# Kernel tuning notes

Hardware: AMD Instinct MI355X
Metric: run time of the kernel (lower is better)

## Reference

```python
import jax, jax.numpy as jnp
import numpy as np

H, M, K, V, F, L = 8, 1024, 128, 128, 4096, 6
B, Q, T = 4, 1024, 1024
EPS = 1e-5


def layer_norm(x, g, b):
    mu = jnp.mean(x, axis=-1, keepdims=True)
    var = jnp.var(x, axis=-1, keepdims=True)
    return (x - mu) * jax.lax.rsqrt(var + EPS) * g + b


def mha(qinput, kvinput, qmask, tmask, qtmask, wq, wk, wv, wo):
    # qinput: bqm, kvinput: btm, masks 1 = ignore
    logits_mask = jnp.maximum(tmask[:, None, :], qtmask)  # bqt
    query = jnp.einsum('hmd,bqm->bhqd', wq, qinput)
    key = jnp.einsum('hmd,btm->bhtd', wk, kvinput)
    val = jnp.einsum('hmd,btm->bhtd', wv, kvinput)
    alogit = jnp.einsum('bhqd,bhtd->bhqt', query, key) + logits_mask[:, None] * -1e6
    att = jax.nn.softmax(alogit * (1.0 / np.sqrt(K)), axis=3)
    pre = jnp.einsum('bhqt,bhtd->bhqd', att, val)
    out = jnp.einsum('hdm,bhqd->bqm', wo, pre)
    return out * (1.0 - qmask[:, :, None])


def ffn(x, qmask, w1, b1, w2, b2):
    s = jax.nn.relu(jnp.einsum('mf,bqm->bqf', w1, x) + b1)
    out = jnp.einsum('fm,bqf->bqm', w2, s) + b2
    return out * (1.0 - qmask[:, :, None])


def setup_inputs() -> dict:
    key = jax.random.key(0)
    ks = jax.random.split(key, 16)
    mscale, fscale, vscale = M ** -0.5, F ** -0.5, V ** -0.5
    d = {
        'enc_out': jax.random.normal(ks[0], (B, T, M), jnp.float32),
        'x': jax.random.normal(ks[1], (B, Q, M), jnp.float32),
        'position_mask': jnp.zeros((B, Q), jnp.float32),
        'qt_self_mask': jnp.broadcast_to(
            (jnp.arange(Q)[:, None] < jnp.arange(Q)[None, :]).astype(jnp.float32),
            (B, Q, Q)),
        'qt_cross_mask': jnp.zeros((B, Q, T), jnp.float32),
        # self-attention params, stacked over layers
        'swq': jax.random.normal(ks[2], (L, H, M, K), jnp.float32) * mscale,
        'swk': jax.random.normal(ks[3], (L, H, M, K), jnp.float32) * mscale,
        'swv': jax.random.normal(ks[4], (L, H, M, V), jnp.float32) * mscale,
        'swo': jax.random.normal(ks[5], (L, H, V, M), jnp.float32) * vscale,
        # cross-attention params
        'cwq': jax.random.normal(ks[6], (L, H, M, K), jnp.float32) * mscale,
        'cwk': jax.random.normal(ks[7], (L, H, M, K), jnp.float32) * mscale,
        'cwv': jax.random.normal(ks[8], (L, H, M, V), jnp.float32) * mscale,
        'cwo': jax.random.normal(ks[9], (L, H, V, M), jnp.float32) * vscale,
        # FFN params
        'w1': jax.random.normal(ks[10], (L, M, F), jnp.float32) * mscale,
        'b1': jnp.zeros((L, F), jnp.float32),
        'w2': jax.random.normal(ks[11], (L, F, M), jnp.float32) * fscale,
        'b2': jnp.zeros((L, M), jnp.float32),
        # LayerNorm params
        'ln1_g': jnp.ones((L, M), jnp.float32), 'ln1_b': jnp.zeros((L, M), jnp.float32),
        'ln2_g': jnp.ones((L, M), jnp.float32), 'ln2_b': jnp.zeros((L, M), jnp.float32),
        'ln3_g': jnp.ones((L, M), jnp.float32), 'ln3_b': jnp.zeros((L, M), jnp.float32),
    }
    return d


def reference(enc_out, x, position_mask, qt_self_mask, qt_cross_mask,
              swq, swk, swv, swo, cwq, cwk, cwv, cwo,
              w1, b1, w2, b2, ln1_g, ln1_b, ln2_g, ln2_b, ln3_g, ln3_b):
    zeros_t = jnp.zeros((enc_out.shape[0], enc_out.shape[1]), x.dtype)
    h = x
    for l in range(L):
        n1 = layer_norm(h, ln1_g[l], ln1_b[l])
        a1 = mha(n1, n1, position_mask, position_mask, qt_self_mask,
                 swq[l], swk[l], swv[l], swo[l])
        h1 = h + a1
        n2 = layer_norm(h1, ln2_g[l], ln2_b[l])
        a2 = mha(n2, enc_out, position_mask, zeros_t, qt_cross_mask,
                 cwq[l], cwk[l], cwv[l], cwo[l])
        h2 = h1 + a2
        n3 = layer_norm(h2, ln3_g[l], ln3_b[l])
        h = h2 + ffn(n3, position_mask, w1[l], b1[l], w2[l], b2[l])
    return h
```

## Files before the change

kernel.cpp:

```cpp
#include <hip/hip_runtime.h>
#include <math.h>

#define NL 6
#define NH 8
#define MD 1024
#define HD 128
#define FF 4096
#define NB 4
#define NQ 1024
#define NT 1024
#define ROWS (NB*NQ)

typedef __attribute__((ext_vector_type(8))) short bf16x8;
typedef __attribute__((ext_vector_type(4))) float f32x4;

__device__ __forceinline__ unsigned short f2bf(float f) {
    unsigned int u = __float_as_uint(f);
    u += 0x7fffu + ((u >> 16) & 1u);
    return (unsigned short)(u >> 16);
}

__device__ __forceinline__ void load16_lds(const unsigned short* g, unsigned short* l) {
    __builtin_amdgcn_global_load_lds(
        (const __attribute__((address_space(1))) unsigned int*)g,
        (__attribute__((address_space(3))) unsigned int*)l, 16, 0, 0);
}

__global__ __launch_bounds__(256) void ln_kernel(
    const float* __restrict__ x, unsigned short* __restrict__ y,
    const float* __restrict__ g, const float* __restrict__ b)
{
    __shared__ float sdata[8];
    int row = blockIdx.x;
    int tid = threadIdx.x;
    const float* xr = x + (size_t)row * MD;
    float4 v = ((const float4*)xr)[tid];
    float s = v.x + v.y + v.z + v.w;
    #pragma unroll
    for (int o = 32; o > 0; o >>= 1) s += __shfl_down(s, o, 64);
    if ((tid & 63) == 0) sdata[tid >> 6] = s;
    __syncthreads();
    if (tid == 0) sdata[4] = sdata[0] + sdata[1] + sdata[2] + sdata[3];
    __syncthreads();
    float mean = sdata[4] * (1.0f / MD);
    float4 d = make_float4(v.x - mean, v.y - mean, v.z - mean, v.w - mean);
    float sq = d.x*d.x + d.y*d.y + d.z*d.z + d.w*d.w;
    #pragma unroll
    for (int o = 32; o > 0; o >>= 1) sq += __shfl_down(sq, o, 64);
    __syncthreads();
    if ((tid & 63) == 0) sdata[tid >> 6] = sq;
    __syncthreads();
    if (tid == 0) sdata[4] = sdata[0] + sdata[1] + sdata[2] + sdata[3];
    __syncthreads();
    float var = sdata[4] * (1.0f / MD);
    float rstd = rsqrtf(var + 1e-5f);
    float4 g4 = ((const float4*)g)[tid];
    float4 b4 = ((const float4*)b)[tid];
    ushort4 o;
    o.x = f2bf(d.x * rstd * g4.x + b4.x);
    o.y = f2bf(d.y * rstd * g4.y + b4.y);
    o.z = f2bf(d.z * rstd * g4.z + b4.z);
    o.w = f2bf(d.w * rstd * g4.w + b4.w);
    *(ushort4*)(y + (size_t)row * MD + tid * 4) = o;
}

__global__ __launch_bounds__(256) void cast_bf16(
    const float* __restrict__ x, unsigned short* __restrict__ y)
{
    int i = blockIdx.x * 256 + threadIdx.x;
    float4 v = ((const float4*)x)[i];
    ushort4 o;
    o.x = f2bf(v.x); o.y = f2bf(v.y); o.z = f2bf(v.z); o.w = f2bf(v.w);
    ((ushort4*)y)[i] = o;
}

__global__ __launch_bounds__(256) void transpose_cast(
    const float* __restrict__ X, unsigned short* __restrict__ Y, int R, int C)
{
    __shared__ float tile[32][33];
    int bz = blockIdx.z;
    int r0 = blockIdx.y * 32, c0 = blockIdx.x * 32;
    const float* Xb = X + (size_t)bz * R * C;
    unsigned short* Yb = Y + (size_t)bz * R * C;
    int tx = threadIdx.x & 31, ty = threadIdx.x >> 5;
    #pragma unroll
    for (int i = 0; i < 4; i++)
        tile[ty + i*8][tx] = Xb[(size_t)(r0 + ty + i*8) * C + c0 + tx];
    __syncthreads();
    #pragma unroll
    for (int i = 0; i < 4; i++)
        Yb[(size_t)(c0 + ty + i*8) * R + r0 + tx] = f2bf(tile[tx][ty + i*8]);
}

#define BKK 64
#define ASZ (128 * BKK)

__device__ __forceinline__ void stage_tiles(
    unsigned short* As, unsigned short* Bs,
    const unsigned short* __restrict__ A, int lda,
    const unsigned short* __restrict__ BT, int ldb,
    int row0, int col0, int kt)
{
    int tid = threadIdx.x;
    #pragma unroll
    for (int it = 0; it < 4; it++) {
        int idx = it * 256 + tid;
        int r = idx >> 3, c = (idx & 7) * 8;
        load16_lds(A + (size_t)(row0 + r) * lda + kt + c, &As[idx * 8]);
    }
    #pragma unroll
    for (int it = 0; it < 4; it++) {
        int idx = it * 256 + tid;
        int r = idx >> 3, c = (idx & 7) * 8;
        load16_lds(BT + (size_t)(col0 + r) * ldb + kt + c, &Bs[idx * 8]);
    }
}

__device__ __forceinline__ void gemm_body(
    unsigned short* As, unsigned short* Bs,
    const unsigned short* __restrict__ A, int lda,
    const unsigned short* __restrict__ BT, int ldb,
    void* __restrict__ Cout, int ldc, int Kdim, int flags,
    const float* __restrict__ bias, int row0, int col0)
{
    int tid = threadIdx.x;
    int lane = tid & 63;
    int wave = tid >> 6;
    int mr = (wave & 1) * 64;
    int nc = (wave >> 1) * 64;
    int lr = lane & 15;
    int quad = lane >> 4;

    f32x4 acc[4][4];
    #pragma unroll
    for (int i = 0; i < 4; i++)
        #pragma unroll
        for (int j = 0; j < 4; j++) acc[i][j] = (f32x4)0.0f;

    const int NKi = Kdim >> 6;
    stage_tiles(As, Bs, A, lda, BT, ldb, row0, col0, 0);
    __syncthreads();

    for (int k = 0; k < NKi; k++) {
        unsigned short* cA = As + (k & 1) * ASZ;
        unsigned short* cB = Bs + (k & 1) * ASZ;
        if (k + 1 < NKi)
            stage_tiles(As + ((k + 1) & 1) * ASZ, Bs + ((k + 1) & 1) * ASZ,
                        A, lda, BT, ldb, row0, col0, (k + 1) * BKK);
        #pragma unroll
        for (int ks = 0; ks < 2; ks++) {
            bf16x8 af[4], bfr[4];
            #pragma unroll
            for (int i = 0; i < 4; i++)
                af[i] = *(const bf16x8*)&cA[(mr + i*16 + lr) * BKK + ks*32 + quad*8];
            #pragma unroll
            for (int j = 0; j < 4; j++)
                bfr[j] = *(const bf16x8*)&cB[(nc + j*16 + lr) * BKK + ks*32 + quad*8];
            #pragma unroll
            for (int i = 0; i < 4; i++)
                #pragma unroll
                for (int j = 0; j < 4; j++)
                    acc[i][j] = __builtin_amdgcn_mfma_f32_16x16x32_bf16(
                        af[i], bfr[j], acc[i][j], 0, 0, 0);
        }
        __syncthreads();
    }

    float bvj[4];
    if (flags & 4) {
        #pragma unroll
        for (int j = 0; j < 4; j++) bvj[j] = bias[col0 + nc + j*16 + lr];
    } else {
        #pragma unroll
        for (int j = 0; j < 4; j++) bvj[j] = 0.0f;
    }

    if (flags & 1) {
        unsigned short* V = (unsigned short*)Cout;
        #pragma unroll
        for (int i = 0; i < 4; i++) {
            int grow0 = row0 + mr + i*16 + quad*4;
            int bb = grow0 >> 10, tt = grow0 & 1023;
            #pragma unroll
            for (int j = 0; j < 4; j++) {
                int gcol = col0 + nc + j*16 + lr;
                int hh = gcol >> 7, dd = gcol & 127;
                ushort4 pk;
                pk.x = f2bf(acc[i][j][0]); pk.y = f2bf(acc[i][j][1]);
                pk.z = f2bf(acc[i][j][2]); pk.w = f2bf(acc[i][j][3]);
                *(ushort4*)(V + (((size_t)(bb*NH + hh)*HD + dd) * NT + tt)) = pk;
            }
        }
    } else if (flags & 2) {
        float* Cf = (float*)Cout;
        #pragma unroll
        for (int i = 0; i < 4; i++) {
            int grow0 = row0 + mr + i*16 + quad*4;
            #pragma unroll
            for (int j = 0; j < 4; j++) {
                int gcol = col0 + nc + j*16 + lr;
                #pragma unroll
                for (int r = 0; r < 4; r++) {
                    float v = acc[i][j][r] + bvj[j];
                    atomicAdd(&Cf[(size_t)(grow0 + r) * ldc + gcol], v);
                }
            }
        }
    } else {
        unsigned short* Cb = (unsigned short*)Cout;
        #pragma unroll
        for (int i = 0; i < 4; i++) {
            int grow0 = row0 + mr + i*16 + quad*4;
            #pragma unroll
            for (int j = 0; j < 4; j++) {
                int gcol = col0 + nc + j*16 + lr;
                #pragma unroll
                for (int r = 0; r < 4; r++) {
                    float v = acc[i][j][r] + bvj[j];
                    if (flags & 8) v = fmaxf(v, 0.0f);
                    Cb[(size_t)(grow0 + r) * ldc + gcol] = f2bf(v);
                }
            }
        }
    }
}

__global__ __launch_bounds__(256) void gemm_bf16(
    const unsigned short* __restrict__ A, int lda,
    const unsigned short* __restrict__ BT, int ldb,
    void* __restrict__ Cout, int ldc, int Kper, int flags,
    const float* __restrict__ bias)
{
    __shared__ unsigned short As[2 * ASZ];
    __shared__ unsigned short Bs[2 * ASZ];
    int row0 = blockIdx.y * 128, col0 = blockIdx.x * 128;
    int kbase = blockIdx.z * Kper;
    if (blockIdx.z) flags &= ~4;
    gemm_body(As, Bs, A + kbase, lda, BT + kbase, ldb, Cout, ldc,
              Kper, flags, bias, row0, col0);
}

__global__ __launch_bounds__(256) void gemm_qkv(
    const unsigned short* __restrict__ Aq,
    const unsigned short* __restrict__ Akv,
    const unsigned short* __restrict__ BTq,
    const unsigned short* __restrict__ BTk,
    const unsigned short* __restrict__ BTv,
    unsigned short* __restrict__ qb,
    unsigned short* __restrict__ kb,
    unsigned short* __restrict__ vbt)
{
    __shared__ unsigned short As[2 * ASZ];
    __shared__ unsigned short Bs[2 * ASZ];
    int w = blockIdx.x >> 3;
    int col0 = (blockIdx.x & 7) * 128;
    int row0 = blockIdx.y * 128;
    const unsigned short* A  = (w == 0) ? Aq : Akv;
    const unsigned short* BT = (w == 0) ? BTq : (w == 1) ? BTk : BTv;
    void* C  = (w == 0) ? (void*)qb : (w == 1) ? (void*)kb : (void*)vbt;
    int flags = (w == 2) ? 1 : 0;
    gemm_body(As, Bs, A, MD, BT, MD, C, MD, MD, flags, nullptr, row0, col0);
}

#define KVB 64

__global__ __launch_bounds__(256) void attn_mfma(
    const unsigned short* __restrict__ qb, const unsigned short* __restrict__ kb,
    const unsigned short* __restrict__ vbt, unsigned short* __restrict__ pr,
    int causal)
{
    __shared__ unsigned short Qs[64 * 136];
    __shared__ unsigned short Ks[64 * 136];
    __shared__ unsigned short Vs[128 * 72];
    __shared__ unsigned short Ps[4 * 16 * 72];

    int tid = threadIdx.x;
    int lane = tid & 63, wave = tid >> 6;
    int lr = lane & 15, quad = lane >> 4;

    int qt, bh;
    if (causal) {
        int bid = blockIdx.x + 16 * blockIdx.y;
        int half = bid >> 8, j = bid & 255;
        qt = half ? (15 - (j & 15)) : (j & 15);
        bh = (half << 4) | (j >> 4);
    } else {
        qt = blockIdx.x; bh = blockIdx.y;
    }
    int b = bh >> 3, h = bh & 7;
    int q0 = qt * 64;
    const float scale = 0.08838834764831845f;

    const unsigned short* kbase = kb + (size_t)(b * NT) * MD + h * HD;
    const unsigned short* vbase = vbt + (size_t)((b * NH + h) * HD) * NT;

    uint4 kreg[4], vreg[4];
    #pragma unroll
    for (int it = 0; it < 4; it++) {
        int idx = it * 256 + tid;
        int r = idx >> 4, c = (idx & 15) * 8;
        kreg[it] = *(const uint4*)(kbase + (size_t)r * MD + c);
    }
    #pragma unroll
    for (int it = 0; it < 4; it++) {
        int idx = it * 256 + tid;
        int r = idx >> 3, c = (idx & 7) * 8;
        vreg[it] = *(const uint4*)(vbase + (size_t)r * NT + c);
    }

    #pragma unroll
    for (int it = 0; it < 4; it++) {
        int idx = it * 256 + tid;
        int r = idx >> 4, c = (idx & 15) * 8;
        *(uint4*)&Qs[r * 136 + c] =
            *(const uint4*)(qb + (size_t)(b*NQ + q0 + r) * MD + h*HD + c);
    }
    __syncthreads();
    bf16x8 aq[4];
    #pragma unroll
    for (int dk = 0; dk < 4; dk++)
        aq[dk] = *(const bf16x8*)&Qs[(wave*16 + lr) * 136 + dk*32 + quad*8];

    f32x4 acc[8];
    #pragma unroll
    for (int n = 0; n < 8; n++) acc[n] = (f32x4)0.0f;
    float m_run[4], l_run[4];
    #pragma unroll
    for (int r = 0; r < 4; r++) { m_run[r] = -1e30f; l_run[r] = 0.0f; }

    unsigned short* Pw = &Ps[wave * 16 * 72];
    int nch = causal ? (qt + 1) : (NT / KVB);
    int grow_base = q0 + wave*16 + quad*4;

    for (int tc = 0; tc < nch; tc++) {
        __syncthreads();
        #pragma unroll
        for (int it = 0; it < 4; it++) {
            int idx = it * 256 + tid;
            int r = idx >> 4, c = (idx & 15) * 8;
            *(uint4*)&Ks[r * 136 + c] = kreg[it];
        }
        #pragma unroll
        for (int it = 0; it < 4; it++) {
            int idx = it * 256 + tid;
            int r = idx >> 3, c = (idx & 7) * 8;
            *(uint4*)&Vs[r * 72 + c] = vreg[it];
        }
        if (tc + 1 < nch) {
            int t0n = (tc + 1) * KVB;
            #pragma unroll
            for (int it = 0; it < 4; it++) {
                int idx = it * 256 + tid;
                int r = idx >> 4, c = (idx & 15) * 8;
                kreg[it] = *(const uint4*)(kbase + (size_t)(t0n + r) * MD + c);
            }
            #pragma unroll
            for (int it = 0; it < 4; it++) {
                int idx = it * 256 + tid;
                int r = idx >> 3, c = (idx & 7) * 8;
                vreg[it] = *(const uint4*)(vbase + (size_t)r * NT + t0n + c);
            }
        }
        __syncthreads();

        int t0 = tc * KVB;

        f32x4 s[4];
        #pragma unroll
        for (int kt = 0; kt < 4; kt++) s[kt] = (f32x4)0.0f;
        __builtin_amdgcn_s_setprio(1);
        #pragma unroll
        for (int dk = 0; dk < 4; dk++) {
            #pragma unroll
            for (int kt = 0; kt < 4; kt++) {
                bf16x8 bk = *(const bf16x8*)&Ks[(kt*16 + lr) * 136 + dk*32 + quad*8];
                s[kt] = __builtin_amdgcn_mfma_f32_16x16x32_bf16(aq[dk], bk, s[kt], 0, 0, 0);
            }
        }
        __builtin_amdgcn_s_setprio(0);

        #pragma unroll
        for (int r = 0; r < 4; r++) {
            float v[4];
            #pragma unroll
            for (int kt = 0; kt < 4; kt++) {
                float x = s[kt][r] * scale;
                if (causal && (t0 + kt*16 + lr > grow_base + r)) x = -1e30f;
                v[kt] = x;
            }
            float mx = fmaxf(fmaxf(v[0], v[1]), fmaxf(v[2], v[3]));
            #pragma unroll
            for (int off = 1; off < 16; off <<= 1)
                mx = fmaxf(mx, __shfl_xor(mx, off));
            mx = fmaxf(mx, m_run[r]);
            float alpha = __expf(m_run[r] - mx);
            float psum = 0.0f;
            #pragma unroll
            for (int kt = 0; kt < 4; kt++) {
                float p = __expf(v[kt] - mx);
                Pw[(quad*4 + r) * 72 + kt*16 + lr] = f2bf(p);
                psum += p;
            }
            #pragma unroll
            for (int off = 1; off < 16; off <<= 1)
                psum += __shfl_xor(psum, off);
            l_run[r] = l_run[r] * alpha + psum;
            m_run[r] = mx;
            #pragma unroll
            for (int n = 0; n < 8; n++) acc[n][r] *= alpha;
        }

        bf16x8 ap0 = *(const bf16x8*)&Pw[lr * 72 + quad * 8];
        bf16x8 ap1 = *(const bf16x8*)&Pw[lr * 72 + 32 + quad * 8];
        __builtin_amdgcn_s_setprio(1);
        #pragma unroll
        for (int n = 0; n < 8; n++) {
            bf16x8 bv0 = *(const bf16x8*)&Vs[(n*16 + lr) * 72 + quad * 8];
            bf16x8 bv1 = *(const bf16x8*)&Vs[(n*16 + lr) * 72 + 32 + quad * 8];
            acc[n] = __builtin_amdgcn_mfma_f32_16x16x32_bf16(ap0, bv0, acc[n], 0, 0, 0);
            acc[n] = __builtin_amdgcn_mfma_f32_16x16x32_bf16(ap1, bv1, acc[n], 0, 0, 0);
        }
        __builtin_amdgcn_s_setprio(0);
    }

    float linv[4];
    #pragma unroll
    for (int r = 0; r < 4; r++) linv[r] = 1.0f / l_run[r];
    #pragma unroll
    for (int n = 0; n < 8; n++) {
        int gcol = h*HD + n*16 + lr;
        #pragma unroll
        for (int r = 0; r < 4; r++) {
            int grow = q0 + wave*16 + quad*4 + r;
            pr[(size_t)(b*NQ + grow) * MD + gcol] = f2bf(acc[n][r] * linv[r]);
        }
    }
}

extern "C" void kernel_launch(void* const* d_in, const int* in_sizes, int n_in,
                              void* d_out, int out_size, void* d_ws, size_t ws_size,
                              hipStream_t stream)
{
    const float* enc  = (const float*)d_in[0];
    const float* x    = (const float*)d_in[1];
    const float* swq  = (const float*)d_in[5];
    const float* swk  = (const float*)d_in[6];
    const float* swv  = (const float*)d_in[7];
    const float* swo  = (const float*)d_in[8];
    const float* cwq  = (const float*)d_in[9];
    const float* cwk  = (const float*)d_in[10];
    const float* cwv  = (const float*)d_in[11];
    const float* cwo  = (const float*)d_in[12];
    const float* w1   = (const float*)d_in[13];
    const float* b1   = (const float*)d_in[14];
    const float* w2   = (const float*)d_in[15];
    const float* b2   = (const float*)d_in[16];
    const float* ln1g = (const float*)d_in[17];
    const float* ln1b = (const float*)d_in[18];
    const float* ln2g = (const float*)d_in[19];
    const float* ln2b = (const float*)d_in[20];
    const float* ln3g = (const float*)d_in[21];
    const float* ln3b = (const float*)d_in[22];

    float* h = (float*)d_out;
    unsigned short* u = (unsigned short*)d_ws;
    const size_t MW = 1024 * 1024;
    unsigned short* nb   = u;
    unsigned short* encb = u + 4*MW;
    unsigned short* qb   = u + 8*MW;
    unsigned short* kb   = u + 12*MW;
    unsigned short* vbt  = u + 16*MW;
    unsigned short* pr   = u + 20*MW;
    unsigned short* sb   = qb;
    unsigned short* wb   = u + 24*MW;

    bool upfront = ws_size >= (size_t)240 * MW;

    hipMemcpyAsync(h, x, 4*MW*sizeof(float), hipMemcpyDeviceToDevice, stream);

    dim3 tb(256);
    cast_bf16<<<4096, tb, 0, stream>>>(enc, encb);

    if (upfront) {
        transpose_cast<<<dim3(4,32,48),  tb, 0, stream>>>(swq, wb + 0*MW,  1024, 128);
        transpose_cast<<<dim3(4,32,48),  tb, 0, stream>>>(swk, wb + 6*MW,  1024, 128);
        transpose_cast<<<dim3(4,32,48),  tb, 0, stream>>>(swv, wb + 12*MW, 1024, 128);
        transpose_cast<<<dim3(32,32,6),  tb, 0, stream>>>(swo, wb + 18*MW, 1024, 1024);
        transpose_cast<<<dim3(4,32,48),  tb, 0, stream>>>(cwq, wb + 24*MW, 1024, 128);
        transpose_cast<<<dim3(4,32,48),  tb, 0, stream>>>(cwk, wb + 30*MW, 1024, 128);
        transpose_cast<<<dim3(4,32,48),  tb, 0, stream>>>(cwv, wb + 36*MW, 1024, 128);
        transpose_cast<<<dim3(32,32,6),  tb, 0, stream>>>(cwo, wb + 42*MW, 1024, 1024);
        transpose_cast<<<dim3(128,32,6), tb, 0, stream>>>(w1,  wb + 48*MW, 1024, 4096);
        transpose_cast<<<dim3(32,128,6), tb, 0, stream>>>(w2,  wb + 72*MW, 4096, 1024);
    }

    dim3 gQKV(24, 32), gO(8, 32, 2), gF1(32, 32), gF2(8, 32, 2), gA(16, 32);

    for (int l = 0; l < NL; l++) {
        unsigned short *pwq, *pwk, *pwv, *pwo, *pcq, *pck, *pcv, *pco, *pw1, *pw2;
        if (upfront) {
            pwq = wb + 0*MW  + l*MW;  pwk = wb + 6*MW  + l*MW;
            pwv = wb + 12*MW + l*MW;  pwo = wb + 18*MW + l*MW;
            pcq = wb + 24*MW + l*MW;  pck = wb + 30*MW + l*MW;
            pcv = wb + 36*MW + l*MW;  pco = wb + 42*MW + l*MW;
            pw1 = wb + 48*MW + l*4*MW; pw2 = wb + 72*MW + l*4*MW;
        } else {
            pwq = wb;        pwk = wb + 1*MW; pwv = wb + 2*MW; pwo = wb + 3*MW;
            pcq = wb + 4*MW; pck = wb + 5*MW; pcv = wb + 6*MW; pco = wb + 7*MW;
            pw1 = wb + 8*MW; pw2 = wb + 12*MW;
            transpose_cast<<<dim3(4,32,8),   tb, 0, stream>>>(swq + l*MW,   pwq, 1024, 128);
            transpose_cast<<<dim3(4,32,8),   tb, 0, stream>>>(swk + l*MW,   pwk, 1024, 128);
            transpose_cast<<<dim3(4,32,8),   tb, 0, stream>>>(swv + l*MW,   pwv, 1024, 128);
            transpose_cast<<<dim3(32,32,1),  tb, 0, stream>>>(swo + l*MW,   pwo, 1024, 1024);
            transpose_cast<<<dim3(4,32,8),   tb, 0, stream>>>(cwq + l*MW,   pcq, 1024, 128);
            transpose_cast<<<dim3(4,32,8),   tb, 0, stream>>>(cwk + l*MW,   pck, 1024, 128);
            transpose_cast<<<dim3(4,32,8),   tb, 0, stream>>>(cwv + l*MW,   pcv, 1024, 128);
            transpose_cast<<<dim3(32,32,1),  tb, 0, stream>>>(cwo + l*MW,   pco, 1024, 1024);
            transpose_cast<<<dim3(128,32,1), tb, 0, stream>>>(w1 + l*4*MW,  pw1, 1024, 4096);
            transpose_cast<<<dim3(32,128,1), tb, 0, stream>>>(w2 + l*4*MW,  pw2, 4096, 1024);
        }

        ln_kernel<<<ROWS, tb, 0, stream>>>(h, nb, ln1g + l*MD, ln1b + l*MD);
        gemm_qkv<<<gQKV, tb, 0, stream>>>(nb, nb, pwq, pwk, pwv, qb, kb, vbt);
        attn_mfma<<<gA, tb, 0, stream>>>(qb, kb, vbt, pr, 1);
        gemm_bf16<<<gO, tb, 0, stream>>>(pr, MD, pwo, MD, h, MD, 512, 2, nullptr);

        ln_kernel<<<ROWS, tb, 0, stream>>>(h, nb, ln2g + l*MD, ln2b + l*MD);
        gemm_qkv<<<gQKV, tb, 0, stream>>>(nb, encb, pcq, pck, pcv, qb, kb, vbt);
        attn_mfma<<<gA, tb, 0, stream>>>(qb, kb, vbt, pr, 0);
        gemm_bf16<<<gO, tb, 0, stream>>>(pr, MD, pco, MD, h, MD, 512, 2, nullptr);

        ln_kernel<<<ROWS, tb, 0, stream>>>(h, nb, ln3g + l*MD, ln3b + l*MD);
        gemm_bf16<<<gF1, tb, 0, stream>>>(nb, MD, pw1, MD, sb, FF, 1024, 4 | 8, b1 + l*FF);
        gemm_bf16<<<gF2, tb, 0, stream>>>(sb, FF, pw2, FF, h, MD, 2048, 2 | 4, b2 + l*MD);
    }
}
```

Before: 3.416 ms.

## Swizzle attention LDS tiles, load Q directly, and skip softmax rescale lazily

```diff
diff --git a/kernel.cpp b/kernel.cpp
--- a/kernel.cpp
+++ b/kernel.cpp
@@ -269,10 +269,9 @@
     const unsigned short* __restrict__ vbt, unsigned short* __restrict__ pr,
     int causal)
 {
-    __shared__ unsigned short Qs[64 * 136];
-    __shared__ unsigned short Ks[64 * 136];
-    __shared__ unsigned short Vs[128 * 72];
-    __shared__ unsigned short Ps[4 * 16 * 72];
+    __shared__ unsigned short Ks[64 * 128];
+    __shared__ unsigned short Vs[128 * 64];
+    __shared__ unsigned short Ps[4 * 16 * 64];
 
     int tid = threadIdx.x;
     int lane = tid & 63, wave = tid >> 6;
@@ -308,18 +307,12 @@
         vreg[it] = *(const uint4*)(vbase + (size_t)r * NT + c);
     }
 
-    #pragma unroll
-    for (int it = 0; it < 4; it++) {
-        int idx = it * 256 + tid;
-        int r = idx >> 4, c = (idx & 15) * 8;
-        *(uint4*)&Qs[r * 136 + c] =
-            *(const uint4*)(qb + (size_t)(b*NQ + q0 + r) * MD + h*HD + c);
-    }
-    __syncthreads();
+    const unsigned short* qrow_p =
+        qb + (size_t)(b*NQ + q0 + wave*16 + lr) * MD + h*HD;
     bf16x8 aq[4];
     #pragma unroll
     for (int dk = 0; dk < 4; dk++)
-        aq[dk] = *(const bf16x8*)&Qs[(wave*16 + lr) * 136 + dk*32 + quad*8];
+        aq[dk] = *(const bf16x8*)(qrow_p + dk*32 + quad*8);
 
     f32x4 acc[8];
     #pragma unroll
@@ -328,23 +321,24 @@
     #pragma unroll
     for (int r = 0; r < 4; r++) { m_run[r] = -1e30f; l_run[r] = 0.0f; }
 
-    unsigned short* Pw = &Ps[wave * 16 * 72];
+    unsigned short* Pw = &Ps[wave * 16 * 64];
     int nch = causal ? (qt + 1) : (NT / KVB);
     int grow_base = q0 + wave*16 + quad*4;
+    int swz = (lr & 7) << 3;
 
     for (int tc = 0; tc < nch; tc++) {
         __syncthreads();
         #pragma unroll
         for (int it = 0; it < 4; it++) {
             int idx = it * 256 + tid;
-            int r = idx >> 4, c = (idx & 15) * 8;
-            *(uint4*)&Ks[r * 136 + c] = kreg[it];
+            int r = idx >> 4, c16 = idx & 15;
+            *(uint4*)&Ks[r * 128 + ((c16 * 8) ^ ((r & 7) << 3))] = kreg[it];
         }
         #pragma unroll
         for (int it = 0; it < 4; it++) {
             int idx = it * 256 + tid;
-            int r = idx >> 3, c = (idx & 7) * 8;
-            *(uint4*)&Vs[r * 72 + c] = vreg[it];
+            int r = idx >> 3, c8 = idx & 7;
+            *(uint4*)&Vs[r * 64 + ((c8 * 8) ^ ((r & 7) << 3))] = vreg[it];
         }
         if (tc + 1 < nch) {
             int t0n = (tc + 1) * KVB;
@@ -373,50 +367,67 @@
         for (int dk = 0; dk < 4; dk++) {
             #pragma unroll
             for (int kt = 0; kt < 4; kt++) {
-                bf16x8 bk = *(const bf16x8*)&Ks[(kt*16 + lr) * 136 + dk*32 + quad*8];
+                bf16x8 bk = *(const bf16x8*)
+                    &Ks[(kt*16 + lr) * 128 + ((dk*32 + quad*8) ^ swz)];
                 s[kt] = __builtin_amdgcn_mfma_f32_16x16x32_bf16(aq[dk], bk, s[kt], 0, 0, 0);
             }
         }
         __builtin_amdgcn_s_setprio(0);
 
+        float mxt[4];
         #pragma unroll
         for (int r = 0; r < 4; r++) {
-            float v[4];
             #pragma unroll
             for (int kt = 0; kt < 4; kt++) {
                 float x = s[kt][r] * scale;
                 if (causal && (t0 + kt*16 + lr > grow_base + r)) x = -1e30f;
-                v[kt] = x;
-            }
-            float mx = fmaxf(fmaxf(v[0], v[1]), fmaxf(v[2], v[3]));
+                s[kt][r] = x;
+            }
+            float mx = fmaxf(fmaxf(s[0][r], s[1][r]), fmaxf(s[2][r], s[3][r]));
             #pragma unroll
             for (int off = 1; off < 16; off <<= 1)
                 mx = fmaxf(mx, __shfl_xor(mx, off));
-            mx = fmaxf(mx, m_run[r]);
-            float alpha = __expf(m_run[r] - mx);
+            mxt[r] = mx;
+        }
+        float need = fmaxf(fmaxf(mxt[0]-m_run[0], mxt[1]-m_run[1]),
+                           fmaxf(mxt[2]-m_run[2], mxt[3]-m_run[3]));
+        if (!__all(need <= 8.0f)) {
+            #pragma unroll
+            for (int r = 0; r < 4; r++) {
+                float mx = fmaxf(mxt[r], m_run[r]);
+                float alpha = __expf(m_run[r] - mx);
+                m_run[r] = mx;
+                l_run[r] *= alpha;
+                #pragma unroll
+                for (int n = 0; n < 8; n++) acc[n][r] *= alpha;
+            }
+        }
+        #pragma unroll
+        for (int r = 0; r < 4; r++) {
+            int prow = quad*4 + r;
+            int pswz = (prow & 7) << 3;
             float psum = 0.0f;
             #pragma unroll
             for (int kt = 0; kt < 4; kt++) {
-                float p = __expf(v[kt] - mx);
-                Pw[(quad*4 + r) * 72 + kt*16 + lr] = f2bf(p);
+                float p = __expf(s[kt][r] - m_run[r]);
+                Pw[prow * 64 + ((kt*16 + lr) ^ pswz)] = f2bf(p);
                 psum += p;
             }
             #pragma unroll
             for (int off = 1; off < 16; off <<= 1)
                 psum += __shfl_xor(psum, off);
-            l_run[r] = l_run[r] * alpha + psum;
-            m_run[r] = mx;
-            #pragma unroll
-            for (int n = 0; n < 8; n++) acc[n][r] *= alpha;
-        }
-
-        bf16x8 ap0 = *(const bf16x8*)&Pw[lr * 72 + quad * 8];
-        bf16x8 ap1 = *(const bf16x8*)&Pw[lr * 72 + 32 + quad * 8];
+            l_run[r] += psum;
+        }
+
+        bf16x8 ap0 = *(const bf16x8*)&Pw[lr * 64 + ((quad * 8) ^ swz)];
+        bf16x8 ap1 = *(const bf16x8*)&Pw[lr * 64 + ((32 + quad * 8) ^ swz)];
         __builtin_amdgcn_s_setprio(1);
         #pragma unroll
         for (int n = 0; n < 8; n++) {
-            bf16x8 bv0 = *(const bf16x8*)&Vs[(n*16 + lr) * 72 + quad * 8];
-            bf16x8 bv1 = *(const bf16x8*)&Vs[(n*16 + lr) * 72 + 32 + quad * 8];
+            bf16x8 bv0 = *(const bf16x8*)
+                &Vs[(n*16 + lr) * 64 + ((quad * 8) ^ swz)];
+            bf16x8 bv1 = *(const bf16x8*)
+                &Vs[(n*16 + lr) * 64 + ((32 + quad * 8) ^ swz)];
             acc[n] = __builtin_amdgcn_mfma_f32_16x16x32_bf16(ap0, bv0, acc[n], 0, 0, 0);
             acc[n] = __builtin_amdgcn_mfma_f32_16x16x32_bf16(ap1, bv1, acc[n], 0, 0, 0);
         }
```

Measured after the change: 3.668 ms. 7.4% more time.
